# Performance work log

Measured on AMD Instinct MI355X. Metric: run time of the kernel, lower is better.

Reference implementation:

```python
import jax, jax.numpy as jnp
import numpy as np

H = 64
N_G, E_G = 30000, 60000
N_LG, E_LG = 60000, 60000


def setup_inputs() -> dict:
    key = jax.random.key(0)
    ks = jax.random.split(key, 30)
    rn = lambda k, s, sc=0.05: jax.random.normal(k, s, jnp.float32) * sc
    return {
        "gx": jax.random.normal(ks[0], (N_G, 20), jnp.float32),
        "g_edge_index": jax.random.randint(ks[1], (2, E_G), 0, N_G, jnp.int32),
        "g_edge_attr": jax.random.uniform(ks[2], (E_G, 4), dtype=jnp.float32),
        "lgx": jax.random.normal(ks[3], (N_LG, 5), jnp.float32),
        "lg_edge_index": jax.random.randint(ks[4], (2, E_LG), 0, N_LG, jnp.int32),
        "lg_edge_attr": jax.random.uniform(ks[5], (E_LG, 1), dtype=jnp.float32),
        "adduct": jax.random.normal(ks[6], (3,), jnp.float32),
        "lin0_w": rn(ks[7], (20, H)), "lin0_b": rn(ks[8], (H,)),
        "g_nn_w1": rn(ks[9], (4, H)), "g_nn_b1": rn(ks[10], (H,)),
        "g_nn_w2": rn(ks[11], (H, H * H), 0.01), "g_nn_b2": rn(ks[12], (H * H,), 0.01),
        "g_root": rn(ks[13], (H, H)), "g_bias": rn(ks[14], (H,)),
        "lin0_lg_w": rn(ks[15], (5, H)), "lin0_lg_b": rn(ks[16], (H,)),
        "lg_nn_w1": rn(ks[17], (1, H)), "lg_nn_b1": rn(ks[18], (H,)),
        "lg_nn_w2": rn(ks[19], (H, H * H), 0.01), "lg_nn_b2": rn(ks[20], (H * H,), 0.01),
        "lg_root": rn(ks[21], (H, H)), "lg_bias": rn(ks[22], (H,)),
        "bott_w": rn(ks[23], (H + H + 3, 384)), "bott_b": rn(ks[24], (384,)),
        "lin1_w": rn(ks[25], (384, 384)), "lin1_b": rn(ks[26], (384,)),
        "lin2_w": rn(ks[27], (384, 1)), "lin2_b": rn(ks[28], (1,)),
    }


def _ecc_branch(x_in, edge_index, edge_attr, w1, b1, w2, b2, root, bias, n_iters, num_nodes):
    """N iterations of NNConv(aggr='mean') + ReLU, then sum pool over nodes."""
    src, tgt = edge_index[0], edge_index[1]  # source->target flow (PyG default)
    # edge MLP -> per-edge [in, out] weight (edge_attr is loop-invariant, compute once)
    W = (jax.nn.relu(edge_attr @ w1 + b1) @ w2 + b2).reshape(-1, H, H)  # [E, H, H]
    cnt = jnp.maximum(
        jax.ops.segment_sum(jnp.ones((tgt.shape[0],), x_in.dtype), tgt, num_segments=num_nodes),
        1.0,
    )
    x = x_in
    for _ in range(n_iters):
        msg = jnp.einsum('ei,eio->eo', x[src], W)  # gather + batched matvec
        agg = jax.ops.segment_sum(msg, tgt, num_segments=num_nodes) / cnt[:, None]  # scatter-mean
        x = jax.nn.relu(x @ root + agg + bias)  # root transform + bias (NNConv defaults)
    return x.sum(axis=0)  # sum pooling -> [H]


def reference(gx, g_edge_index, g_edge_attr, lgx, lg_edge_index, lg_edge_attr, adduct,
              lin0_w, lin0_b, g_nn_w1, g_nn_b1, g_nn_w2, g_nn_b2, g_root, g_bias,
              lin0_lg_w, lin0_lg_b, lg_nn_w1, lg_nn_b1, lg_nn_w2, lg_nn_b2, lg_root, lg_bias,
              bott_w, bott_b, lin1_w, lin1_b, lin2_w, lin2_b):
    out_g = _ecc_branch(jax.nn.relu(gx @ lin0_w + lin0_b), g_edge_index, g_edge_attr,
                        g_nn_w1, g_nn_b1, g_nn_w2, g_nn_b2, g_root, g_bias, 3, N_G)
    out_lg = _ecc_branch(jax.nn.relu(lgx @ lin0_lg_w + lin0_lg_b), lg_edge_index, lg_edge_attr,
                         lg_nn_w1, lg_nn_b1, lg_nn_w2, lg_nn_b2, lg_root, lg_bias, 3, N_LG)
    out = jnp.concatenate([out_g, out_lg, adduct], axis=-1)  # [131]
    out = jax.nn.relu(out @ bott_w + bott_b)
    for _ in range(6):
        out = jax.nn.relu(out @ lin1_w + lin1_b)
    return out @ lin2_w + lin2_b  # [1]
```

## Files before the change

kernel.cpp:

```cpp
#include <hip/hip_runtime.h>

typedef unsigned short u16;
using short8_t  = __attribute__((ext_vector_type(8)))  short;
using float16_t = __attribute__((ext_vector_type(16))) float;

#define NKT 260
#define DEG_CAP 32

__device__ __forceinline__ float bf2f(u16 b) { return __uint_as_float(((unsigned)b) << 16); }
__device__ __forceinline__ u16 f2bf(float f) {
  unsigned u = __float_as_uint(f);
  return (u16)((u + 0x7fffu + ((u >> 16) & 1u)) >> 16);
}

union U8 { short8_t s; uint4 v; unsigned u[4]; };

__device__ __forceinline__ short8_t scale8f(const float* xf, float hs) {
  U8 out;
  #pragma unroll
  for (int p = 0; p < 4; ++p) {
    float lo = xf[2 * p] * hs;
    float hi = xf[2 * p + 1] * hs;
    out.u[p] = __builtin_amdgcn_perm(__float_as_uint(hi), __float_as_uint(lo), 0x07060302);
  }
  return out.s;
}

template<int IN>
__device__ __forceinline__ void affine_body(
    const float* __restrict__ Xin, const float* __restrict__ W, const float* __restrict__ Bv,
    u16* __restrict__ Xout, int N, int gid)
{
  int n = gid >> 6, o = gid & 63;
  if (n >= N) return;
  float acc = Bv[o];
  #pragma unroll
  for (int i = 0; i < IN; ++i)
    acc = fmaf(Xin[n * IN + i], W[i * 64 + o], acc);
  Xout[gid] = f2bf(fmaxf(acc, 0.f));
}

__global__ __launch_bounds__(256) void affine_all_kernel(
    const float* __restrict__ gx, const float* __restrict__ l0w, const float* __restrict__ l0b, u16* __restrict__ xg,
    const float* __restrict__ lgx, const float* __restrict__ llw, const float* __restrict__ llb, u16* __restrict__ xl,
    const float* __restrict__ gea, const float* __restrict__ gw1, const float* __restrict__ gb1, u16* __restrict__ hg,
    const float* __restrict__ lea, const float* __restrict__ lw1, const float* __restrict__ lb1, u16* __restrict__ hl,
    int B0, int B1, int B2, int NG, int NLG, int EG, int ELG)
{
  int b = blockIdx.x, t = threadIdx.x;
  if (b < B0)       affine_body<20>(gx, l0w, l0b, xg, NG, b * 256 + t);
  else if (b < B1)  affine_body<5>(lgx, llw, llb, xl, NLG, (b - B0) * 256 + t);
  else if (b < B2)  affine_body<4>(gea, gw1, gb1, hg, EG, (b - B1) * 256 + t);
  else              affine_body<1>(lea, lw1, lb1, hl, ELG, (b - B2) * 256 + t);
}

__device__ __forceinline__ void bpack_body(
    const float* __restrict__ w2, const float* __restrict__ b2, u16* __restrict__ Bp, int gid)
{
  if (gid >= NKT * 128) return;
  int lane = gid & 63;
  int nt = (gid >> 6) & 1;
  int kt = gid >> 7;
  int o = nt * 32 + (lane & 31);
  int kbase = kt * 16 + (lane >> 5) * 8;
  u16 vals[8];
  #pragma unroll
  for (int j = 0; j < 8; ++j) {
    int k = kbase + j;
    vals[j] = f2bf((k < 4096) ? w2[(k >> 6) * 4096 + (k & 63) * 64 + o]
                              : b2[(k - 4096) * 64 + o]);
  }
  uint4 pack;
  pack.x = (unsigned)vals[0] | ((unsigned)vals[1] << 16);
  pack.y = (unsigned)vals[2] | ((unsigned)vals[3] << 16);
  pack.z = (unsigned)vals[4] | ((unsigned)vals[5] << 16);
  pack.w = (unsigned)vals[6] | ((unsigned)vals[7] << 16);
  *(uint4*)(Bp + (size_t)gid * 8) = pack;
}

__device__ __forceinline__ void rootpack_body(const float* __restrict__ root, u16* __restrict__ Rp, int gid)
{
  if (gid >= 512) return;
  int lane = gid & 63;
  int nt = (gid >> 6) & 1;
  int kt = gid >> 7;
  int o = nt * 32 + (lane & 31);
  int kbase = kt * 16 + (lane >> 5) * 8;
  u16 vals[8];
  #pragma unroll
  for (int j = 0; j < 8; ++j) vals[j] = f2bf(root[(kbase + j) * 64 + o]);
  uint4 pack;
  pack.x = (unsigned)vals[0] | ((unsigned)vals[1] << 16);
  pack.y = (unsigned)vals[2] | ((unsigned)vals[3] << 16);
  pack.z = (unsigned)vals[4] | ((unsigned)vals[5] << 16);
  pack.w = (unsigned)vals[6] | ((unsigned)vals[7] << 16);
  *(uint4*)(Rp + (size_t)gid * 8) = pack;
}

__global__ __launch_bounds__(256) void pack_all_kernel(
    const float* __restrict__ gw2, const float* __restrict__ gb2, u16* __restrict__ bpg,
    const float* __restrict__ lw2, const float* __restrict__ lb2, u16* __restrict__ bpl,
    const float* __restrict__ groot, u16* __restrict__ rpg,
    const float* __restrict__ lroot, u16* __restrict__ rpl)
{
  int b = blockIdx.x, t = threadIdx.x;
  if (b < 130)       bpack_body(gw2, gb2, bpg, b * 256 + t);
  else if (b < 260)  bpack_body(lw2, lb2, bpl, (b - 130) * 256 + t);
  else if (b < 262)  rootpack_body(groot, rpg, (b - 260) * 256 + t);
  else               rootpack_body(lroot, rpl, (b - 262) * 256 + t);
}

__device__ __forceinline__ void hist_body(
    const int* __restrict__ eidx, int* __restrict__ cnt, int* __restrict__ elist, int E, int e)
{
  if (e < E) {
    int tg = eidx[E + e];
    int pos = atomicAdd(cnt + tg, 1);
    if (pos < DEG_CAP) elist[(size_t)tg * DEG_CAP + pos] = e;
  }
}

__global__ __launch_bounds__(256) void hist_kernel(
    const int* __restrict__ eig, int* __restrict__ cg, int* __restrict__ elg, int Eg, int nbg,
    const int* __restrict__ eil, int* __restrict__ cl, int* __restrict__ ell, int El)
{
  int b = blockIdx.x, t = threadIdx.x;
  if (b < nbg) hist_body(eig, cg, elg, Eg, b * 256 + t);
  else         hist_body(eil, cl, ell, El, (b - nbg) * 256 + t);
}

__global__ __launch_bounds__(128, 2) void msg_gemm_kernel(
    const u16* __restrict__ Xg, const u16* __restrict__ Hg, const u16* __restrict__ Bg,
    const int* __restrict__ eig, u16* __restrict__ Mg, int Eg, int nbg,
    const u16* __restrict__ Xl, const u16* __restrict__ Hl, const u16* __restrict__ Bl,
    const int* __restrict__ eil, u16* __restrict__ Ml, int El)
{
  const int b = blockIdx.x;
  const u16 *X, *Hh, *Bp; const int* eidx; u16* msg; int E, e0;
  if (b < nbg) { X = Xg; Hh = Hg; Bp = Bg; eidx = eig; msg = Mg; E = Eg; e0 = b * 128; }
  else         { X = Xl; Hh = Hl; Bp = Bl; eidx = eil; msg = Ml; E = El; e0 = (b - nbg) * 128; }

  const int t = threadIdx.x;
  const int lane = t & 63;
  const int wid = t >> 6;
  const int ml = lane & 31;
  const int q  = lane >> 5;

  const int ea = e0 + wid * 64 + ml;
  const int eb = ea + 32;
  const int eac = ea < E ? ea : E - 1;
  const int ebc = eb < E ? eb : E - 1;
  const int sa = eidx[eac], sb = eidx[ebc];

  float xfa[4][8], xfb[4][8];
  {
    const u16* xpa = X + (size_t)sa * 64 + q * 8;
    const u16* xpb = X + (size_t)sb * 64 + q * 8;
    #pragma unroll
    for (int s = 0; s < 4; ++s) {
      U8 va, vb;
      va.v = *(const uint4*)(xpa + s * 16);
      vb.v = *(const uint4*)(xpb + s * 16);
      #pragma unroll
      for (int p = 0; p < 4; ++p) {
        xfa[s][2 * p]     = __uint_as_float(va.u[p] << 16);
        xfa[s][2 * p + 1] = __uint_as_float(va.u[p] & 0xffff0000u);
        xfb[s][2 * p]     = __uint_as_float(vb.u[p] << 16);
        xfb[s][2 * p + 1] = __uint_as_float(vb.u[p] & 0xffff0000u);
      }
    }
  }

  const uint4* ha4 = (const uint4*)(Hh + (size_t)eac * 64);
  const uint4* hb4 = (const uint4*)(Hh + (size_t)ebc * 64);
  uint4 hc0 = ha4[0], hn0 = ha4[1];
  uint4 hc1 = hb4[0], hn1 = hb4[1];

  const uint4* bpv = (const uint4*)Bp;
  uint4 rb0[4], rb1[4];
  #pragma unroll
  for (int p = 0; p < 4; ++p) {
    rb0[p] = bpv[p * 128 + lane];
    rb1[p] = bpv[p * 128 + 64 + lane];
  }

  float16_t acc00, acc01, acc10, acc11;
  #pragma unroll
  for (int i = 0; i < 16; ++i) { acc00[i] = 0.f; acc01[i] = 0.f; acc10[i] = 0.f; acc11[i] = 0.f; }

  for (int blk = 0; blk < 8; ++blk) {
    #pragma unroll
    for (int j = 0; j < 8; ++j) {
      unsigned w0 = ((const unsigned*)&hc0)[j >> 1];
      unsigned w1 = ((const unsigned*)&hc1)[j >> 1];
      float hs0 = bf2f((u16)((j & 1) ? (w0 >> 16) : (w0 & 0xffffu)));
      float hs1 = bf2f((u16)((j & 1) ? (w1 >> 16) : (w1 & 0xffffu)));
      #pragma unroll
      for (int tt = 0; tt < 4; ++tt) {
        int kt = ((blk * 8 + j) << 2) + tt;
        U8 b0, b1;
        b0.v = rb0[tt]; b1.v = rb1[tt];
        rb0[tt] = bpv[(kt + 4) * 128 + lane];
        rb1[tt] = bpv[(kt + 4) * 128 + 64 + lane];
        short8_t a0 = scale8f(xfa[tt], hs0);
        short8_t a1 = scale8f(xfb[tt], hs1);
        acc00 = __builtin_amdgcn_mfma_f32_32x32x16_bf16(a0, b0.s, acc00, 0, 0, 0);
        acc01 = __builtin_amdgcn_mfma_f32_32x32x16_bf16(a0, b1.s, acc01, 0, 0, 0);
        acc10 = __builtin_amdgcn_mfma_f32_32x32x16_bf16(a1, b0.s, acc10, 0, 0, 0);
        acc11 = __builtin_amdgcn_mfma_f32_32x32x16_bf16(a1, b1.s, acc11, 0, 0, 0);
      }
    }
    hc0 = hn0; hc1 = hn1;
    if (blk < 6) { hn0 = ha4[blk + 2]; hn1 = hb4[blk + 2]; }
  }
  #pragma unroll
  for (int tt = 0; tt < 4; ++tt) {
    U8 b0, b1;
    b0.v = rb0[tt]; b1.v = rb1[tt];
    short8_t a0 = scale8f(xfa[tt], 1.0f);
    short8_t a1 = scale8f(xfb[tt], 1.0f);
    acc00 = __builtin_amdgcn_mfma_f32_32x32x16_bf16(a0, b0.s, acc00, 0, 0, 0);
    acc01 = __builtin_amdgcn_mfma_f32_32x32x16_bf16(a0, b1.s, acc01, 0, 0, 0);
    acc10 = __builtin_amdgcn_mfma_f32_32x32x16_bf16(a1, b0.s, acc10, 0, 0, 0);
    acc11 = __builtin_amdgcn_mfma_f32_32x32x16_bf16(a1, b1.s, acc11, 0, 0, 0);
  }

  #pragma unroll
  for (int reg = 0; reg < 16; ++reg) {
    int row = (reg & 3) + 8 * (reg >> 2) + 4 * q;
    int e1 = e0 + wid * 64 + row;
    int e2 = e1 + 32;
    if (e1 < E) {
      msg[(size_t)e1 * 64 + ml]      = f2bf(acc00[reg]);
      msg[(size_t)e1 * 64 + 32 + ml] = f2bf(acc01[reg]);
    }
    if (e2 < E) {
      msg[(size_t)e2 * 64 + ml]      = f2bf(acc10[reg]);
      msg[(size_t)e2 * 64 + 32 + ml] = f2bf(acc11[reg]);
    }
  }
}

__global__ __launch_bounds__(256, 4) void update_kernel(
    const u16* __restrict__ Xig, const u16* __restrict__ Mgg, const int* __restrict__ cg,
    const int* __restrict__ elg, const u16* __restrict__ rpg, const float* __restrict__ bg,
    u16* __restrict__ Xog, int Ng, int nbg,
    const u16* __restrict__ Xil, const u16* __restrict__ Mgl, const int* __restrict__ cl,
    const int* __restrict__ ell, const u16* __restrict__ rpl, const float* __restrict__ bl,
    u16* __restrict__ Xol, int Nl)
{
  const int b = blockIdx.x;
  const u16 *Xin, *rootp, *msg; const float *bias; const int *cnt, *elist;
  u16* Xout; int N, n0;
  if (b < nbg) { Xin=Xig; msg=Mgg; cnt=cg; elist=elg; rootp=rpg; bias=bg; Xout=Xog; N=Ng; n0=b*128; }
  else         { Xin=Xil; msg=Mgl; cnt=cl; elist=ell; rootp=rpl; bias=bl; Xout=Xol; N=Nl; n0=(b-nbg)*128; }

  const int t = threadIdx.x;
  const int lane = t & 63;
  const int wid = t >> 6;
  const int ml = lane & 31;
  const int q  = lane >> 5;
  const int nbase = n0 + wid * 32;

  const int na = nbase + ml;
  const int nac = na < N ? na : N - 1;

  U8 xr[4];
  {
    const u16* xp = Xin + (size_t)nac * 64 + q * 8;
    #pragma unroll
    for (int s = 0; s < 4; ++s) xr[s].v = *(const uint4*)(xp + s * 16);
  }
  U8 rp[8];
  {
    const uint4* rpv = (const uint4*)rootp;
    #pragma unroll
    for (int i = 0; i < 8; ++i) rp[i].v = rpv[i * 64 + lane];
  }
  const float bias0 = bias[ml], bias1 = bias[32 + ml];

  float16_t acc0, acc1;
  #pragma unroll
  for (int i = 0; i < 16; ++i) { acc0[i] = 0.f; acc1[i] = 0.f; }
  #pragma unroll
  for (int kt = 0; kt < 4; ++kt) {
    acc0 = __builtin_amdgcn_mfma_f32_32x32x16_bf16(xr[kt].s, rp[kt * 2 + 0].s, acc0, 0, 0, 0);
    acc1 = __builtin_amdgcn_mfma_f32_32x32x16_bf16(xr[kt].s, rp[kt * 2 + 1].s, acc1, 0, 0, 0);
  }

  #pragma unroll
  for (int reg = 0; reg < 16; ++reg) {
    int row = (reg & 3) + 8 * (reg >> 2) + 4 * q;
    int nn = nbase + row;
    if (nn < N) {
      int c = cnt[nn];
      int cc = c < DEG_CAP ? c : DEG_CAP;
      const int* ep = elist + (size_t)nn * DEG_CAP;
      float a0 = 0.f, a1 = 0.f;
      int j = 0;
      for (; j + 4 <= cc; j += 4) {
        int e0i = ep[j], e1i = ep[j + 1], e2i = ep[j + 2], e3i = ep[j + 3];
        u16 m00 = msg[(size_t)e0i * 64 + ml], m01 = msg[(size_t)e0i * 64 + 32 + ml];
        u16 m10 = msg[(size_t)e1i * 64 + ml], m11 = msg[(size_t)e1i * 64 + 32 + ml];
        u16 m20 = msg[(size_t)e2i * 64 + ml], m21 = msg[(size_t)e2i * 64 + 32 + ml];
        u16 m30 = msg[(size_t)e3i * 64 + ml], m31 = msg[(size_t)e3i * 64 + 32 + ml];
        a0 += bf2f(m00) + bf2f(m10) + bf2f(m20) + bf2f(m30);
        a1 += bf2f(m01) + bf2f(m11) + bf2f(m21) + bf2f(m31);
      }
      for (; j < cc; ++j) {
        int e = ep[j];
        a0 += bf2f(msg[(size_t)e * 64 + ml]);
        a1 += bf2f(msg[(size_t)e * 64 + 32 + ml]);
      }
      float rc = (c > 1) ? (1.0f / (float)c) : 1.0f;
      float o0 = fmaxf(acc0[reg] + a0 * rc + bias0, 0.f);
      float o1 = fmaxf(acc1[reg] + a1 * rc + bias1, 0.f);
      Xout[(size_t)nn * 64 + ml]      = f2bf(o0);
      Xout[(size_t)nn * 64 + 32 + ml] = f2bf(o1);
    }
  }
}

__device__ __forceinline__ void pool_body(const u16* __restrict__ X, float* __restrict__ out64,
                                          int nchunks, int bid, int t)
{
  __shared__ float red[64];
  if (t < 64) red[t] = 0.f;
  __syncthreads();
  int gid = bid * 256 + t;
  float s[8];
  #pragma unroll
  for (int j = 0; j < 8; ++j) s[j] = 0.f;
  for (int i = gid; i < nchunks; i += 256 * 256) {
    uint4 v = ((const uint4*)X)[i];
    s[0] += bf2f((u16)(v.x & 0xffffu)); s[1] += bf2f((u16)(v.x >> 16));
    s[2] += bf2f((u16)(v.y & 0xffffu)); s[3] += bf2f((u16)(v.y >> 16));
    s[4] += bf2f((u16)(v.z & 0xffffu)); s[5] += bf2f((u16)(v.z >> 16));
    s[6] += bf2f((u16)(v.w & 0xffffu)); s[7] += bf2f((u16)(v.w >> 16));
  }
  int cg = (gid & 7) * 8;
  #pragma unroll
  for (int j = 0; j < 8; ++j) atomicAdd(red + cg + j, s[j]);
  __syncthreads();
  if (t < 64) atomicAdd(out64 + t, red[t]);
}

__global__ __launch_bounds__(256) void pool_kernel(
    const u16* __restrict__ Xg, float* __restrict__ og, int ncg,
    const u16* __restrict__ Xl, float* __restrict__ ol, int ncl)
{
  int b = blockIdx.x, t = threadIdx.x;
  if (b < 256) pool_body(Xg, og, ncg, b, t);
  else         pool_body(Xl, ol, ncl, b - 256, t);
}

__global__ __launch_bounds__(256) void prep_head_kernel(
    const float* __restrict__ pg, const float* __restrict__ plg, const float* __restrict__ adduct,
    float* __restrict__ v)
{
  int t = threadIdx.x;
  if (t < 131) v[t] = (t < 64) ? pg[t] : (t < 128 ? plg[t - 64] : adduct[t - 128]);
}

__global__ __launch_bounds__(256) void gemv_relu_kernel(
    const float* __restrict__ in, const float* __restrict__ W, const float* __restrict__ b,
    float* __restrict__ out, int Ni, int No)
{
  __shared__ float red[16][17];
  int t = threadIdx.x;
  int ol = t & 15, ig = t >> 4;
  int o = blockIdx.x * 16 + ol;
  float s = 0.f;
  for (int i = ig; i < Ni; i += 16)
    s = fmaf(in[i], W[i * No + o], s);
  red[ig][ol] = s;
  __syncthreads();
  if (t < 16) {
    int oo = blockIdx.x * 16 + t;
    float acc = b[oo];
    #pragma unroll
    for (int g = 0; g < 16; ++g) acc += red[g][t];
    out[oo] = fmaxf(acc, 0.f);
  }
}

__global__ __launch_bounds__(384) void final_kernel(
    const float* __restrict__ u, const float* __restrict__ l2w, const float* __restrict__ l2b,
    float* __restrict__ out)
{
  __shared__ float wred[6];
  int t = threadIdx.x;
  float p = u[t] * l2w[t];
  #pragma unroll
  for (int off = 32; off > 0; off >>= 1) p += __shfl_down(p, off);
  if ((t & 63) == 0) wred[t >> 6] = p;
  __syncthreads();
  if (t == 0) {
    float s = l2b[0];
    #pragma unroll
    for (int i = 0; i < 6; ++i) s += wred[i];
    out[0] = s;
  }
}

extern "C" void kernel_launch(void* const* d_in, const int* in_sizes, int n_in,
                              void* d_out, int out_size, void* d_ws, size_t ws_size,
                              hipStream_t stream)
{
  const int NG = 30000, EG = 60000, NLG = 60000, ELG = 60000;

  const float* gx      = (const float*)d_in[0];
  const int*   g_ei    = (const int*)  d_in[1];
  const float* g_ea    = (const float*)d_in[2];
  const float* lgx     = (const float*)d_in[3];
  const int*   lg_ei   = (const int*)  d_in[4];
  const float* lg_ea   = (const float*)d_in[5];
  const float* adduct  = (const float*)d_in[6];
  const float* lin0_w  = (const float*)d_in[7];
  const float* lin0_b  = (const float*)d_in[8];
  const float* g_w1    = (const float*)d_in[9];
  const float* g_b1    = (const float*)d_in[10];
  const float* g_w2    = (const float*)d_in[11];
  const float* g_b2    = (const float*)d_in[12];
  const float* g_root  = (const float*)d_in[13];
  const float* g_bias  = (const float*)d_in[14];
  const float* l0lg_w  = (const float*)d_in[15];
  const float* l0lg_b  = (const float*)d_in[16];
  const float* lg_w1   = (const float*)d_in[17];
  const float* lg_b1   = (const float*)d_in[18];
  const float* lg_w2   = (const float*)d_in[19];
  const float* lg_b2   = (const float*)d_in[20];
  const float* lg_root = (const float*)d_in[21];
  const float* lg_bias = (const float*)d_in[22];
  const float* bott_w  = (const float*)d_in[23];
  const float* bott_b  = (const float*)d_in[24];
  const float* lin1_w  = (const float*)d_in[25];
  const float* lin1_b  = (const float*)d_in[26];
  const float* lin2_w  = (const float*)d_in[27];
  const float* lin2_b  = (const float*)d_in[28];

  char* p = (char*)d_ws;
  auto alloc = [&](size_t bytes) { char* r = p; p += (bytes + 255) & ~(size_t)255; return r; };
  u16*   xg_a   = (u16*)  alloc((size_t)NG  * 64 * 2);
  u16*   xg_b   = (u16*)  alloc((size_t)NG  * 64 * 2);
  u16*   xl_a   = (u16*)  alloc((size_t)NLG * 64 * 2);
  u16*   xl_b   = (u16*)  alloc((size_t)NLG * 64 * 2);
  u16*   h_g    = (u16*)  alloc((size_t)EG  * 64 * 2);
  u16*   h_l    = (u16*)  alloc((size_t)ELG * 64 * 2);
  u16*   bp_g   = (u16*)  alloc((size_t)NKT * 128 * 8 * 2 + 16384);
  u16*   bp_l   = (u16*)  alloc((size_t)NKT * 128 * 8 * 2 + 16384);
  u16*   rp_g   = (u16*)  alloc(512 * 8 * 2);
  u16*   rp_l   = (u16*)  alloc(512 * 8 * 2);
  u16*   msg_g  = (u16*)  alloc((size_t)EG  * 64 * 2);
  u16*   msg_l  = (u16*)  alloc((size_t)ELG * 64 * 2);
  int*   cnt_g  = (int*)  alloc((size_t)NG  * 4);
  int*   cnt_l  = (int*)  alloc((size_t)NLG * 4);
  int*   el_g   = (int*)  alloc((size_t)NG  * DEG_CAP * 4);
  int*   el_l   = (int*)  alloc((size_t)NLG * DEG_CAP * 4);
  float* pool_g = (float*)alloc(64 * 4);
  float* pool_l = (float*)alloc(64 * 4);
  float* hv     = (float*)alloc(131 * 4);
  float* h0     = (float*)alloc(384 * 4);
  float* h1     = (float*)alloc(384 * 4);

  const int B0 = NG * 64 / 256, B1 = B0 + NLG * 64 / 256, B2 = B1 + EG * 64 / 256;
  const int Btot = B2 + ELG * 64 / 256;
  affine_all_kernel<<<Btot, 256, 0, stream>>>(
      gx, lin0_w, lin0_b, xg_a, lgx, l0lg_w, l0lg_b, xl_a,
      g_ea, g_w1, g_b1, h_g, lg_ea, lg_w1, lg_b1, h_l,
      B0, B1, B2, NG, NLG, EG, ELG);
  pack_all_kernel<<<264, 256, 0, stream>>>(g_w2, g_b2, bp_g, lg_w2, lg_b2, bp_l,
                                           g_root, rp_g, lg_root, rp_l);
  hipMemsetAsync(cnt_g, 0, (size_t)((char*)cnt_l - (char*)cnt_g) + (size_t)NLG * 4, stream);
  const int nhg = (EG + 255) / 256, nhl = (ELG + 255) / 256;
  hist_kernel<<<nhg + nhl, 256, 0, stream>>>(g_ei, cnt_g, el_g, EG, nhg, lg_ei, cnt_l, el_l, ELG);

  const int nbg_m = (EG + 127) / 128, nbl_m = (ELG + 127) / 128;
  const int nbg_u = (NG + 127) / 128, nbl_u = (NLG + 127) / 128;
  u16 *xgc = xg_a, *xgn = xg_b, *xlc = xl_a, *xln = xl_b;
  for (int it = 0; it < 3; ++it) {
    msg_gemm_kernel<<<nbg_m + nbl_m, 128, 0, stream>>>(
        xgc, h_g, bp_g, g_ei, msg_g, EG, nbg_m,
        xlc, h_l, bp_l, lg_ei, msg_l, ELG);
    update_kernel<<<nbg_u + nbl_u, 256, 0, stream>>>(
        xgc, msg_g, cnt_g, el_g, rp_g, g_bias, xgn, NG, nbg_u,
        xlc, msg_l, cnt_l, el_l, rp_l, lg_bias, xln, NLG);
    u16* tmp = xgc; xgc = xgn; xgn = tmp;
    tmp = xlc; xlc = xln; xln = tmp;
  }

  hipMemsetAsync(pool_g, 0, (size_t)((char*)pool_l - (char*)pool_g) + 64 * 4, stream);
  pool_kernel<<<512, 256, 0, stream>>>(xgc, pool_g, NG * 8, xlc, pool_l, NLG * 8);

  prep_head_kernel<<<1, 256, 0, stream>>>(pool_g, pool_l, adduct, hv);
  gemv_relu_kernel<<<24, 256, 0, stream>>>(hv, bott_w, bott_b, h0, 131, 384);
  float* ua = h0; float* ub = h1;
  for (int L = 0; L < 6; ++L) {
    gemv_relu_kernel<<<24, 256, 0, stream>>>(ua, lin1_w, lin1_b, ub, 384, 384);
    float* tmp = ua; ua = ub; ub = tmp;
  }
  final_kernel<<<1, 384, 0, stream>>>(ua, lin2_w, lin2_b, (float*)d_out);
}
```

Before: 503.8 us.

## Stage packed edge-weight tiles in double-buffered LDS via direct global-to-LDS loads

The message GEMM previously had each wave stream the packed W2 basis tiles from global memory into registers and compute two 32-edge tiles. It now uses 256-thread blocks whose four waves each handle 32 edges, while the 4096-element basis chunks are loaded cooperatively into a double-buffered LDS tile with global_load_lds. This is meant to cut redundant global and L2 traffic for the shared basis matrix and lower register pressure so more waves can be resident. The cost is a __syncthreads per chunk (65 barriers) and half as much MFMA work per wave between barriers.

```diff
diff --git a/kernel.cpp b/kernel.cpp
--- a/kernel.cpp
+++ b/kernel.cpp
@@ -129,12 +129,14 @@
   else         hist_body(eil, cl, ell, El, (b - nbg) * 256 + t);
 }
 
-__global__ __launch_bounds__(128, 2) void msg_gemm_kernel(
+__global__ __launch_bounds__(256, 4) void msg_gemm_kernel(
     const u16* __restrict__ Xg, const u16* __restrict__ Hg, const u16* __restrict__ Bg,
     const int* __restrict__ eig, u16* __restrict__ Mg, int Eg, int nbg,
     const u16* __restrict__ Xl, const u16* __restrict__ Hl, const u16* __restrict__ Bl,
     const int* __restrict__ eil, u16* __restrict__ Ml, int El)
 {
+  __shared__ __align__(16) u16 sB[2][4096];
+
   const int b = blockIdx.x;
   const u16 *X, *Hh, *Bp; const int* eidx; u16* msg; int E, e0;
   if (b < nbg) { X = Xg; Hh = Hg; Bp = Bg; eidx = eig; msg = Mg; E = Eg; e0 = b * 128; }
@@ -146,97 +148,93 @@
   const int ml = lane & 31;
   const int q  = lane >> 5;
 
-  const int ea = e0 + wid * 64 + ml;
-  const int eb = ea + 32;
+  {
+    const u16* src = Bp + (size_t)wid * 1024 + (size_t)lane * 8;
+    u16* dst = &sB[0][wid * 1024];
+    __builtin_amdgcn_global_load_lds((const __attribute__((address_space(1))) void*)src,
+                                     (__attribute__((address_space(3))) void*)dst, 16, 0, 0);
+    __builtin_amdgcn_global_load_lds((const __attribute__((address_space(1))) void*)(src + 512),
+                                     (__attribute__((address_space(3))) void*)(dst + 512), 16, 0, 0);
+  }
+
+  const int ea  = e0 + wid * 32 + ml;
   const int eac = ea < E ? ea : E - 1;
-  const int ebc = eb < E ? eb : E - 1;
-  const int sa = eidx[eac], sb = eidx[ebc];
-
-  float xfa[4][8], xfb[4][8];
+  const int sa  = eidx[eac];
+
+  float xfa[4][8];
   {
-    const u16* xpa = X + (size_t)sa * 64 + q * 8;
-    const u16* xpb = X + (size_t)sb * 64 + q * 8;
+    const u16* xp = X + (size_t)sa * 64 + q * 8;
     #pragma unroll
     for (int s = 0; s < 4; ++s) {
-      U8 va, vb;
-      va.v = *(const uint4*)(xpa + s * 16);
-      vb.v = *(const uint4*)(xpb + s * 16);
+      U8 va;
+      va.v = *(const uint4*)(xp + s * 16);
       #pragma unroll
       for (int p = 0; p < 4; ++p) {
         xfa[s][2 * p]     = __uint_as_float(va.u[p] << 16);
         xfa[s][2 * p + 1] = __uint_as_float(va.u[p] & 0xffff0000u);
-        xfb[s][2 * p]     = __uint_as_float(vb.u[p] << 16);
-        xfb[s][2 * p + 1] = __uint_as_float(vb.u[p] & 0xffff0000u);
       }
     }
   }
 
   const uint4* ha4 = (const uint4*)(Hh + (size_t)eac * 64);
-  const uint4* hb4 = (const uint4*)(Hh + (size_t)ebc * 64);
-  uint4 hc0 = ha4[0], hn0 = ha4[1];
-  uint4 hc1 = hb4[0], hn1 = hb4[1];
-
-  const uint4* bpv = (const uint4*)Bp;
-  uint4 rb0[4], rb1[4];
-  #pragma unroll
-  for (int p = 0; p < 4; ++p) {
-    rb0[p] = bpv[p * 128 + lane];
-    rb1[p] = bpv[p * 128 + 64 + lane];
-  }
-
-  float16_t acc00, acc01, acc10, acc11;
-  #pragma unroll
-  for (int i = 0; i < 16; ++i) { acc00[i] = 0.f; acc01[i] = 0.f; acc10[i] = 0.f; acc11[i] = 0.f; }
-
-  for (int blk = 0; blk < 8; ++blk) {
+  uint4 hcur = ha4[0], hnext = ha4[1];
+
+  float16_t acc0, acc1;
+  #pragma unroll
+  for (int i = 0; i < 16; ++i) { acc0[i] = 0.f; acc1[i] = 0.f; }
+
+  const uint4* sb0 = (const uint4*)&sB[0][0];
+  const uint4* sb1 = (const uint4*)&sB[1][0];
+
+  __syncthreads();
+
+  for (int g = 0; g < 8; ++g) {
     #pragma unroll
-    for (int j = 0; j < 8; ++j) {
-      unsigned w0 = ((const unsigned*)&hc0)[j >> 1];
-      unsigned w1 = ((const unsigned*)&hc1)[j >> 1];
-      float hs0 = bf2f((u16)((j & 1) ? (w0 >> 16) : (w0 & 0xffffu)));
-      float hs1 = bf2f((u16)((j & 1) ? (w1 >> 16) : (w1 & 0xffffu)));
+    for (int cc = 0; cc < 8; ++cc) {
+      const int c = g * 8 + cc;
+      {
+        const u16* src = Bp + (size_t)(c + 1) * 4096 + (size_t)wid * 1024 + (size_t)lane * 8;
+        u16* dst = &sB[(cc + 1) & 1][wid * 1024];
+        __builtin_amdgcn_global_load_lds((const __attribute__((address_space(1))) void*)src,
+                                         (__attribute__((address_space(3))) void*)dst, 16, 0, 0);
+        __builtin_amdgcn_global_load_lds((const __attribute__((address_space(1))) void*)(src + 512),
+                                         (__attribute__((address_space(3))) void*)(dst + 512), 16, 0, 0);
+      }
+      unsigned hw = ((const unsigned*)&hcur)[cc >> 1];
+      float hs = bf2f((u16)((cc & 1) ? (hw >> 16) : (hw & 0xffffu)));
+      const uint4* sb = (cc & 1) ? sb1 : sb0;
       #pragma unroll
       for (int tt = 0; tt < 4; ++tt) {
-        int kt = ((blk * 8 + j) << 2) + tt;
         U8 b0, b1;
-        b0.v = rb0[tt]; b1.v = rb1[tt];
-        rb0[tt] = bpv[(kt + 4) * 128 + lane];
-        rb1[tt] = bpv[(kt + 4) * 128 + 64 + lane];
-        short8_t a0 = scale8f(xfa[tt], hs0);
-        short8_t a1 = scale8f(xfb[tt], hs1);
-        acc00 = __builtin_amdgcn_mfma_f32_32x32x16_bf16(a0, b0.s, acc00, 0, 0, 0);
-        acc01 = __builtin_amdgcn_mfma_f32_32x32x16_bf16(a0, b1.s, acc01, 0, 0, 0);
-        acc10 = __builtin_amdgcn_mfma_f32_32x32x16_bf16(a1, b0.s, acc10, 0, 0, 0);
-        acc11 = __builtin_amdgcn_mfma_f32_32x32x16_bf16(a1, b1.s, acc11, 0, 0, 0);
+        b0.v = sb[tt * 128 + lane];
+        b1.v = sb[tt * 128 + 64 + lane];
+        short8_t a0 = scale8f(xfa[tt], hs);
+        acc0 = __builtin_amdgcn_mfma_f32_32x32x16_bf16(a0, b0.s, acc0, 0, 0, 0);
+        acc1 = __builtin_amdgcn_mfma_f32_32x32x16_bf16(a0, b1.s, acc1, 0, 0, 0);
       }
+      __syncthreads();
     }
-    hc0 = hn0; hc1 = hn1;
-    if (blk < 6) { hn0 = ha4[blk + 2]; hn1 = hb4[blk + 2]; }
-  }
+    hcur = hnext;
+    if (g < 6) hnext = ha4[g + 2];
+  }
+
   #pragma unroll
   for (int tt = 0; tt < 4; ++tt) {
     U8 b0, b1;
-    b0.v = rb0[tt]; b1.v = rb1[tt];
+    b0.v = sb0[tt * 128 + lane];
+    b1.v = sb0[tt * 128 + 64 + lane];
     short8_t a0 = scale8f(xfa[tt], 1.0f);
-    short8_t a1 = scale8f(xfb[tt], 1.0f);
-    acc00 = __builtin_amdgcn_mfma_f32_32x32x16_bf16(a0, b0.s, acc00, 0, 0, 0);
-    acc01 = __builtin_amdgcn_mfma_f32_32x32x16_bf16(a0, b1.s, acc01, 0, 0, 0);
-    acc10 = __builtin_amdgcn_mfma_f32_32x32x16_bf16(a1, b0.s, acc10, 0, 0, 0);
-    acc11 = __builtin_amdgcn_mfma_f32_32x32x16_bf16(a1, b1.s, acc11, 0, 0, 0);
+    acc0 = __builtin_amdgcn_mfma_f32_32x32x16_bf16(a0, b0.s, acc0, 0, 0, 0);
+    acc1 = __builtin_amdgcn_mfma_f32_32x32x16_bf16(a0, b1.s, acc1, 0, 0, 0);
   }
 
   #pragma unroll
   for (int reg = 0; reg < 16; ++reg) {
     int row = (reg & 3) + 8 * (reg >> 2) + 4 * q;
-    int e1 = e0 + wid * 64 + row;
-    int e2 = e1 + 32;
+    int e1 = e0 + wid * 32 + row;
     if (e1 < E) {
-      msg[(size_t)e1 * 64 + ml]      = f2bf(acc00[reg]);
-      msg[(size_t)e1 * 64 + 32 + ml] = f2bf(acc01[reg]);
-    }
-    if (e2 < E) {
-      msg[(size_t)e2 * 64 + ml]      = f2bf(acc10[reg]);
-      msg[(size_t)e2 * 64 + 32 + ml] = f2bf(acc11[reg]);
+      msg[(size_t)e1 * 64 + ml]      = f2bf(acc0[reg]);
+      msg[(size_t)e1 * 64 + 32 + ml] = f2bf(acc1[reg]);
     }
   }
 }
@@ -479,7 +477,7 @@
   const int nbg_u = (NG + 127) / 128, nbl_u = (NLG + 127) / 128;
   u16 *xgc = xg_a, *xgn = xg_b, *xlc = xl_a, *xln = xl_b;
   for (int it = 0; it < 3; ++it) {
-    msg_gemm_kernel<<<nbg_m + nbl_m, 128, 0, stream>>>(
+    msg_gemm_kernel<<<nbg_m + nbl_m, 256, 0, stream>>>(
         xgc, h_g, bp_g, g_ei, msg_g, EG, nbg_m,
         xlc, h_l, bp_l, lg_ei, msg_l, ELG);
     update_kernel<<<nbg_u + nbl_u, 256, 0, stream>>>(
```

Measured after the change: 509.6 us. Within noise of the previous version (+1.1%).
